# Kernel tuning notes

Hardware: AMD Instinct MI355X
Metric: run time of the kernel (lower is better)

## Reference

```python
import jax, jax.numpy as jnp
import numpy as np

# 8 corner offsets for neighborhood_size=1: lower and lower+1 in each dim
_OFFSETS = jnp.array([[dx, dy, dz] for dx in (0, 1) for dy in (0, 1) for dz in (0, 1)], dtype=jnp.int32)  # (8,3)


def setup_inputs() -> dict:
    key = jax.random.key(0)
    k1, k2 = jax.random.split(key)
    B, N, C, D = 4, 32768, 128, 32
    ptcloud = jax.random.uniform(k1, (B, N, 3), dtype=jnp.float32, minval=-1.0, maxval=1.0)
    cubic_features = jax.random.normal(k2, (B, C, D, D, D), dtype=jnp.float32)
    return {"ptcloud": ptcloud, "cubic_features": cubic_features}


def reference(ptcloud, cubic_features):
    # ptcloud: (B,N,3) in [-1,1]; cubic_features: (B,C,Dx,Dy,Dz)
    B, C, Dx, Dy, Dz = cubic_features.shape
    dims = jnp.array([Dx, Dy, Dz], dtype=jnp.int32)
    scaling = (jnp.array([Dx, Dy, Dz], dtype=jnp.float32) - 1.0) * 0.5
    p = (ptcloud + 1.0) * scaling  # (B,N,3) in voxel coords
    lower = jnp.floor(p).astype(jnp.int32)  # (B,N,3)
    idx = lower[:, :, None, :] + _OFFSETS[None, None, :, :]  # (B,N,8,3)
    valid = jnp.all((idx >= 0) & (idx < dims), axis=-1)  # (B,N,8)
    idx_c = jnp.clip(idx, 0, dims - 1)
    flat = (idx_c[..., 0] * Dy + idx_c[..., 1]) * Dz + idx_c[..., 2]  # (B,N,8)
    feats = cubic_features.reshape(B, C, Dx * Dy * Dz)  # (B,C,V)
    # gather: indices broadcast over channel axis -> (B,C,N*8)
    gathered = jnp.take_along_axis(feats, flat.reshape(B, 1, -1), axis=2)
    gathered = gathered.reshape(B, C, ptcloud.shape[1], 8).transpose(0, 2, 3, 1)  # (B,N,8,C)
    return gathered * valid[..., None].astype(gathered.dtype)
```

## Files before the change

### kernel.cpp

```cpp
#include <hip/hip_runtime.h>

#define B_ 4
#define N_ 32768
#define C_ 128
#define D_ 32
#define V_ (D_ * D_ * D_)

__global__ __launch_bounds__(256) void transpose_kernel(
    const float* __restrict__ in,
    float* __restrict__ out)
{
    __shared__ float tile[32][33];
    const int b  = blockIdx.z;
    const int v0 = blockIdx.x * 32;
    const int c0 = blockIdx.y * 32;
    const float* inb  = in  + (size_t)b * C_ * V_;
    float*       outb = out + (size_t)b * C_ * V_;
    const int tx = threadIdx.x;
    const int ty = threadIdx.y;

#pragma unroll
    for (int i = 0; i < 32; i += 8)
        tile[ty + i][tx] = inb[(size_t)(c0 + ty + i) * V_ + (v0 + tx)];

    __syncthreads();

#pragma unroll
    for (int i = 0; i < 32; i += 8)
        outb[(size_t)(v0 + ty + i) * C_ + (c0 + tx)] = tile[tx][ty + i];
}

__global__ __launch_bounds__(256) void gather_kernel(
    const float* __restrict__ ptcloud,
    const float* __restrict__ featsT,
    float* __restrict__ out)
{
    const int point = blockIdx.x;
    const int b = point >> 15;
    const int t = threadIdx.x;
    const int k  = t >> 5;
    const int c4 = (t & 31) << 2;

    const float* pp = ptcloud + (size_t)point * 3;
    const float s = (D_ - 1) * 0.5f;
    const float fx = (pp[0] + 1.0f) * s;
    const float fy = (pp[1] + 1.0f) * s;
    const float fz = (pp[2] + 1.0f) * s;
    const int lx = (int)floorf(fx);
    const int ly = (int)floorf(fy);
    const int lz = (int)floorf(fz);

    const int ix = lx + (k >> 2);
    const int iy = ly + ((k >> 1) & 1);
    const int iz = lz + (k & 1);
    const bool valid = ((unsigned)ix < (unsigned)D_) &
                       ((unsigned)iy < (unsigned)D_) &
                       ((unsigned)iz < (unsigned)D_);
    const int cx = min(max(ix, 0), D_ - 1);
    const int cy = min(max(iy, 0), D_ - 1);
    const int cz = min(max(iz, 0), D_ - 1);
    const int flat = (cx * D_ + cy) * D_ + cz;

    const float4 v =
        *(const float4*)(featsT + ((size_t)b * V_ + flat) * C_ + c4);
    const float m = valid ? 1.0f : 0.0f;
    float4 r;
    r.x = v.x * m; r.y = v.y * m; r.z = v.z * m; r.w = v.w * m;

    *(float4*)(out + (((size_t)point * 8 + k) * C_) + c4) = r;
}

__global__ __launch_bounds__(128) void gather_direct_kernel(
    const float* __restrict__ ptcloud,
    const float* __restrict__ feats,
    float* __restrict__ out)
{
    const int point = blockIdx.x;
    const int b = point >> 15;
    const int c = threadIdx.x;

    const float* pp = ptcloud + (size_t)point * 3;
    const float s = (D_ - 1) * 0.5f;
    const int lx = (int)floorf((pp[0] + 1.0f) * s);
    const int ly = (int)floorf((pp[1] + 1.0f) * s);
    const int lz = (int)floorf((pp[2] + 1.0f) * s);

    const float* fb = feats + ((size_t)b * C_ + c) * V_;
    float* ob = out + (size_t)point * 8 * C_ + c;

#pragma unroll
    for (int k = 0; k < 8; ++k) {
        const int ix = lx + (k >> 2);
        const int iy = ly + ((k >> 1) & 1);
        const int iz = lz + (k & 1);
        const bool valid = ((unsigned)ix < (unsigned)D_) &
                           ((unsigned)iy < (unsigned)D_) &
                           ((unsigned)iz < (unsigned)D_);
        const int cx = min(max(ix, 0), D_ - 1);
        const int cy = min(max(iy, 0), D_ - 1);
        const int cz = min(max(iz, 0), D_ - 1);
        const int flat = (cx * D_ + cy) * D_ + cz;
        ob[(size_t)k * C_] = fb[flat] * (valid ? 1.0f : 0.0f);
    }
}

extern "C" void kernel_launch(void* const* d_in, const int* in_sizes, int n_in,
                              void* d_out, int out_size, void* d_ws, size_t ws_size,
                              hipStream_t stream) {
    const float* ptcloud = (const float*)d_in[0];
    const float* feats   = (const float*)d_in[1];
    float* out = (float*)d_out;

    const size_t need = (size_t)B_ * C_ * V_ * sizeof(float);
    if (ws_size >= need) {
        float* featsT = (float*)d_ws;
        dim3 tb(32, 8);
        dim3 tg(V_ / 32, C_ / 32, B_);
        transpose_kernel<<<tg, tb, 0, stream>>>(feats, featsT);
        gather_kernel<<<B_ * N_, 256, 0, stream>>>(ptcloud, featsT, out);
    } else {
        gather_direct_kernel<<<B_ * N_, 128, 0, stream>>>(ptcloud, feats, out);
    }
}
```

Measured before the change: 652.8 us.

## Batch four points per gather block and widen transpose to full channel tiles

Result: faster. 607.4 us (-7.0%).

```diff
diff --git a/kernel.cpp b/kernel.cpp
--- a/kernel.cpp
+++ b/kernel.cpp
@@ -6,28 +6,44 @@
 #define D_ 32
 #define V_ (D_ * D_ * D_)
 
+typedef float f4 __attribute__((ext_vector_type(4)));
+
 __global__ __launch_bounds__(256) void transpose_kernel(
     const float* __restrict__ in,
     float* __restrict__ out)
 {
-    __shared__ float tile[32][33];
-    const int b  = blockIdx.z;
+    __shared__ float lds[C_ * 33];
+    const int b  = blockIdx.y;
     const int v0 = blockIdx.x * 32;
-    const int c0 = blockIdx.y * 32;
     const float* inb  = in  + (size_t)b * C_ * V_;
     float*       outb = out + (size_t)b * C_ * V_;
-    const int tx = threadIdx.x;
-    const int ty = threadIdx.y;
+    const int t = threadIdx.x;
 
+    const int vq = t & 7;
+    const int ci = t >> 3;
 #pragma unroll
-    for (int i = 0; i < 32; i += 8)
-        tile[ty + i][tx] = inb[(size_t)(c0 + ty + i) * V_ + (v0 + tx)];
+    for (int r = 0; r < 4; ++r) {
+        const int c = ci + r * 32;
+        const f4 f = __builtin_nontemporal_load(
+            reinterpret_cast<const f4*>(inb + (size_t)c * V_ + v0 + vq * 4));
+        float* d = &lds[c * 33 + vq * 4];
+        d[0] = f.x; d[1] = f.y; d[2] = f.z; d[3] = f.w;
+    }
 
     __syncthreads();
 
+    const int c4 = (t & 31) << 2;
+    const int vr = t >> 5;
 #pragma unroll
-    for (int i = 0; i < 32; i += 8)
-        outb[(size_t)(v0 + ty + i) * C_ + (c0 + tx)] = tile[tx][ty + i];
+    for (int r = 0; r < 4; ++r) {
+        const int v = vr + r * 8;
+        f4 g;
+        g.x = lds[(c4 + 0) * 33 + v];
+        g.y = lds[(c4 + 1) * 33 + v];
+        g.z = lds[(c4 + 2) * 33 + v];
+        g.w = lds[(c4 + 3) * 33 + v];
+        *reinterpret_cast<f4*>(outb + (size_t)(v0 + v) * C_ + c4) = g;
+    }
 }
 
 __global__ __launch_bounds__(256) void gather_kernel(
@@ -35,11 +51,12 @@
     const float* __restrict__ featsT,
     float* __restrict__ out)
 {
-    const int point = blockIdx.x;
-    const int b = point >> 15;
     const int t = threadIdx.x;
-    const int k  = t >> 5;
-    const int c4 = (t & 31) << 2;
+    const int point = (blockIdx.x << 2) + (t >> 6);
+    const int l  = t & 63;
+    const int kk = l >> 5;
+    const int c4 = (l & 31) << 2;
+    const int b  = point >> 15;
 
     const float* pp = ptcloud + (size_t)point * 3;
     const float s = (D_ - 1) * 0.5f;
@@ -50,24 +67,35 @@
     const int ly = (int)floorf(fy);
     const int lz = (int)floorf(fz);
 
-    const int ix = lx + (k >> 2);
-    const int iy = ly + ((k >> 1) & 1);
-    const int iz = lz + (k & 1);
-    const bool valid = ((unsigned)ix < (unsigned)D_) &
-                       ((unsigned)iy < (unsigned)D_) &
-                       ((unsigned)iz < (unsigned)D_);
-    const int cx = min(max(ix, 0), D_ - 1);
-    const int cy = min(max(iy, 0), D_ - 1);
+    const int iz = lz + kk;
+    const bool vz = (unsigned)iz < (unsigned)D_;
     const int cz = min(max(iz, 0), D_ - 1);
-    const int flat = (cx * D_ + cy) * D_ + cz;
 
-    const float4 v =
-        *(const float4*)(featsT + ((size_t)b * V_ + flat) * C_ + c4);
-    const float m = valid ? 1.0f : 0.0f;
-    float4 r;
-    r.x = v.x * m; r.y = v.y * m; r.z = v.z * m; r.w = v.w * m;
+    const float* src = featsT + (size_t)b * V_ * C_ + c4;
+    float* dst = out + ((size_t)point * 8 + kk) * C_ + c4;
 
-    *(float4*)(out + (((size_t)point * 8 + k) * C_) + c4) = r;
+    f4 v[4];
+    float m[4];
+#pragma unroll
+    for (int j = 0; j < 4; ++j) {
+        const int ix = lx + (j >> 1);
+        const int iy = ly + (j & 1);
+        const bool valid = vz &
+                           ((unsigned)ix < (unsigned)D_) &
+                           ((unsigned)iy < (unsigned)D_);
+        const int cx = min(max(ix, 0), D_ - 1);
+        const int cy = min(max(iy, 0), D_ - 1);
+        const int flat = (cx * D_ + cy) * D_ + cz;
+        v[j] = *reinterpret_cast<const f4*>(src + (size_t)flat * C_);
+        m[j] = valid ? 1.0f : 0.0f;
+    }
+
+#pragma unroll
+    for (int j = 0; j < 4; ++j) {
+        f4 r = v[j] * m[j];
+        __builtin_nontemporal_store(
+            r, reinterpret_cast<f4*>(dst + (size_t)(2 * j) * C_));
+    }
 }
 
 __global__ __launch_bounds__(128) void gather_direct_kernel(
@@ -114,10 +142,9 @@
     const size_t need = (size_t)B_ * C_ * V_ * sizeof(float);
     if (ws_size >= need) {
         float* featsT = (float*)d_ws;
-        dim3 tb(32, 8);
-        dim3 tg(V_ / 32, C_ / 32, B_);
-        transpose_kernel<<<tg, tb, 0, stream>>>(feats, featsT);
-        gather_kernel<<<B_ * N_, 256, 0, stream>>>(ptcloud, featsT, out);
+        dim3 tg(V_ / 32, B_);
+        transpose_kernel<<<tg, 256, 0, stream>>>(feats, featsT);
+        gather_kernel<<<(B_ * N_) / 4, 256, 0, stream>>>(ptcloud, featsT, out);
     } else {
         gather_direct_kernel<<<B_ * N_, 128, 0, stream>>>(ptcloud, feats, out);
     }
```
